# Kernel tuning notes

Hardware: AMD Instinct MI355X
Metric: run time of the kernel (lower is better)

## Reference

```python
import jax, jax.numpy as jnp
import numpy as np

B, P, N = 1024, 100, 101
EMB, H, DK = 128, 8, 16
SQRT_EMB = 11.313708498984761
CLIP = 10.0


def setup_inputs() -> dict:
    key = jax.random.key(0)
    ks = jax.random.split(key, 12)
    inp = {
        "encoded_last_node": jax.random.normal(ks[0], (B, P, EMB), jnp.float32),
        "load": jax.random.uniform(ks[1], (B, P), jnp.float32),
        "time": jax.random.uniform(ks[2], (B, P), jnp.float32),
        "length": jax.random.uniform(ks[3], (B, P), jnp.float32),
        "route_open": jax.random.uniform(ks[4], (B, P), jnp.float32),
        "ninf_mask": jnp.zeros((B, P, N), jnp.float32),
        "encoded_nodes": jax.random.normal(ks[5], (B, N, EMB), jnp.float32),
        # weights stored [in, out]
        "Wq": jax.random.normal(ks[6], (EMB + 4, H * DK), jnp.float32) * 0.05,
        "Wk": jax.random.normal(ks[7], (EMB, H * DK), jnp.float32) * 0.05,
        "Wv": jax.random.normal(ks[8], (EMB, H * DK), jnp.float32) * 0.05,
        "Wc": jax.random.normal(ks[9], (H * DK, EMB), jnp.float32) * 0.05,
        "bc": jax.random.normal(ks[10], (EMB,), jnp.float32) * 0.05,
    }
    return inp


def _heads(x):
    # [B, n, H*DK] -> [B, H, n, DK]
    b, n, _ = x.shape
    return x.reshape(b, n, H, DK).transpose(0, 2, 1, 3)


def reference(encoded_last_node, load, time, length, route_open, ninf_mask,
              encoded_nodes, Wq, Wk, Wv, Wc, bc):
    # set_kv
    k = _heads(encoded_nodes @ Wk)            # [B,H,N,DK]
    v = _heads(encoded_nodes @ Wv)            # [B,H,N,DK]
    # forward
    input_cat = jnp.concatenate(
        [encoded_last_node, load[:, :, None], time[:, :, None],
         length[:, :, None], route_open[:, :, None]], axis=2)  # [B,P,EMB+4]
    q = _heads(input_cat @ Wq)                # [B,H,P,DK]
    score = jnp.einsum('bhpd,bhnd->bhpn', q, k) / jnp.sqrt(jnp.float32(DK))
    score = score + ninf_mask[:, None, :, :]
    weights = jax.nn.softmax(score, axis=3)
    out = jnp.einsum('bhpn,bhnd->bhpd', weights, v)
    out_concat = out.transpose(0, 2, 1, 3).reshape(out.shape[0], out.shape[2], H * DK)
    mh = out_concat @ Wc + bc                 # [B,P,EMB]
    score2 = jnp.einsum('bpe,bne->bpn', mh, encoded_nodes) / SQRT_EMB
    score2 = CLIP * jnp.tanh(score2) + ninf_mask
    probs = jax.nn.softmax(score2, axis=2)
    return probs
```

## Files before the change

kernel.cpp:

```cpp
#include <hip/hip_runtime.h>
#include <stdint.h>

#define B_    1024
#define P_    100
#define N_    101
#define EMB_  128
#define H_    8
#define DK_   16

#define ROWS  112
#define KSTR  136

typedef uint16_t bf16;
typedef __attribute__((ext_vector_type(8))) short short8;
typedef __attribute__((ext_vector_type(4))) float float4v;

struct F4 { float x, y, z, w; };

#define L2E 1.4426950408889634f

#if __has_builtin(__builtin_amdgcn_exp2f)
#define EXP2(x) __builtin_amdgcn_exp2f(x)
#else
#define EXP2(x) exp2f(x)
#endif
#if __has_builtin(__builtin_amdgcn_rcpf)
#define RCP(x) __builtin_amdgcn_rcpf(x)
#else
#define RCP(x) (1.0f / (x))
#endif

__device__ __forceinline__ float b2f(bf16 u) {
    union { uint32_t i; float f; } c; c.i = ((uint32_t)u) << 16; return c.f;
}
__device__ __forceinline__ bf16 f2b(float f) {
    union { float f; uint32_t i; } c; c.f = f;
    return (bf16)((c.i + 0x8000u) >> 16);
}
__device__ __forceinline__ uint32_t pk2(float a, float b) {
    union { float f; uint32_t i; } ca, cb; ca.f = a; cb.f = b;
    return __builtin_amdgcn_perm(cb.i + 0x8000u, ca.i + 0x8000u, 0x07060302u);
}

__device__ __forceinline__ void stage_m(const float* __restrict__ src, int nrows,
                                        bf16* __restrict__ dst, int tid) {
    for (int i = tid; i < ROWS * 32; i += 1024) {
        int r = i >> 5, c = (i & 31) << 2;
        uint32_t p0 = 0, p1 = 0;
        if (r < nrows) {
            float4 v = *(const float4*)(src + (size_t)r * EMB_ + c);
            p0 = pk2(v.x, v.y); p1 = pk2(v.z, v.w);
        }
        uint32_t* d = (uint32_t*)(dst + r * KSTR + c);
        d[0] = p0; d[1] = p1;
    }
}

__global__ __launch_bounds__(256)
void prep_wT(const float* __restrict__ Wq, const float* __restrict__ Wk,
             const float* __restrict__ Wv, const float* __restrict__ Wc,
             bf16* __restrict__ ws) {
    int idx = blockIdx.x * 256 + threadIdx.x;
    int w = idx >> 14, rem = idx & 16383;
    int k = rem >> 7, o = rem & 127;
    const float* W = (w == 0) ? Wk : (w == 1) ? Wv : (w == 2) ? Wq : Wc;
    ws[((size_t)w << 14) + o * 128 + k] = f2b(W[(size_t)k * 128 + o]);
}

__global__ __launch_bounds__(1024, 4)
void vrp_kernel(const float* __restrict__ eln,
                const float* __restrict__ load_,
                const float* __restrict__ time_,
                const float* __restrict__ len_,
                const float* __restrict__ open_,
                const float* __restrict__ mask_,
                const float* __restrict__ enc_,
                const float* __restrict__ Wq,
                const float* __restrict__ bc,
                const bf16* __restrict__ wsWT,
                float* __restrict__ out)
{
    const int b    = blockIdx.x;
    const int tid  = threadIdx.x;
    const int wave = tid >> 6;
    const int lane = tid & 63;
    const int lr = lane & 15, lq = lane >> 4, lk = lq << 3;

    __shared__ bf16 smem[78336];
    __shared__ float sS4[ROWS * 4];
    __shared__ float sWq4[4 * EMB_];
    bf16* const R1 = smem;
    bf16* const R2 = smem + 15232;
    bf16* const R3 = smem + 30464;
    bf16* const R4 = smem + 47872;
    bf16* const R5 = smem + 63104;

    const bf16* WkT = wsWT;
    const bf16* WvT = wsWT + 16384;
    const bf16* WqT = wsWT + 32768;
    const bf16* WcT = wsWT + 49152;

    const float* encB  = enc_  + (size_t)b * N_ * EMB_;
    const float* elnB  = eln   + (size_t)b * P_ * EMB_;
    const float* maskB = mask_ + (size_t)b * P_ * N_;
    float*       outB  = out   + (size_t)b * P_ * N_;

    stage_m(encB, N_, R1, tid);
    stage_m(elnB, P_, R5, tid);
    if (tid < 512) {
        int d = tid >> 2, c = 112 + ((tid & 3) << 2);
        uint32_t* z = (uint32_t*)(R3 + d * KSTR + c);
        z[0] = 0; z[1] = 0;
    }
    if (tid < ROWS * 4) {
        int r = tid >> 2, j = tid & 3;
        float v = 0.f;
        if (r < P_) {
            const float* s4 = (j == 0) ? load_ : (j == 1) ? time_
                             : (j == 2) ? len_ : open_;
            v = s4[(size_t)b * P_ + r];
        }
        sS4[r * 4 + j] = v;
    }
    if (tid < 512) {
        int j = tid >> 7, c = tid & 127;
        sWq4[j * EMB_ + c] = Wq[(size_t)(EMB_ + j) * EMB_ + c];
    }
    __syncthreads();

    {
        const int col = 16 * (wave & 7) + lr;
        const int mt0 = (wave >> 3) ? 4 : 0;
        const int mt1 = (wave >> 3) ? 7 : 4;
        short8 bk[4], bv[4], bq[4];
        {
            const bf16* rk = WkT + (size_t)col * 128 + lk;
            const bf16* rv = WvT + (size_t)col * 128 + lk;
            const bf16* rq = WqT + (size_t)col * 128 + lk;
            #pragma unroll
            for (int s = 0; s < 4; ++s) {
                bk[s] = *(const short8*)(rk + s * 32);
                bv[s] = *(const short8*)(rv + s * 32);
                bq[s] = *(const short8*)(rq + s * 32);
            }
        }
        float w0 = sWq4[col], w1 = sWq4[EMB_ + col];
        float w2 = sWq4[2 * EMB_ + col], w3 = sWq4[3 * EMB_ + col];
        for (int mt = mt0; mt < mt1; ++mt) {
            short8 a[4];
            #pragma unroll
            for (int s = 0; s < 4; ++s)
                a[s] = *(const short8*)(R1 + (mt * 16 + lr) * KSTR + s * 32 + lk);
            float4v ck = {0.f, 0.f, 0.f, 0.f}, cv = {0.f, 0.f, 0.f, 0.f};
            #pragma unroll
            for (int s = 0; s < 4; ++s) {
                ck = __builtin_amdgcn_mfma_f32_16x16x32_bf16(a[s], bk[s], ck, 0, 0, 0);
                cv = __builtin_amdgcn_mfma_f32_16x16x32_bf16(a[s], bv[s], cv, 0, 0, 0);
            }
            int n0 = mt * 16 + (lq << 2);
            #pragma unroll
            for (int r = 0; r < 4; ++r)
                R2[(n0 + r) * KSTR + col] = f2b(ck[r]);
            uint32_t* d = (uint32_t*)(R3 + col * KSTR + n0);
            d[0] = pk2(cv[0], cv[1]);
            d[1] = pk2(cv[2], cv[3]);
            short8 aq[4];
            #pragma unroll
            for (int s = 0; s < 4; ++s)
                aq[s] = *(const short8*)(R5 + (mt * 16 + lr) * KSTR + s * 32 + lk);
            float4v cq = {0.f, 0.f, 0.f, 0.f};
            #pragma unroll
            for (int s = 0; s < 4; ++s)
                cq = __builtin_amdgcn_mfma_f32_16x16x32_bf16(aq[s], bq[s], cq, 0, 0, 0);
            int row0 = mt * 16 + (lq << 2);
            #pragma unroll
            for (int r = 0; r < 4; ++r) {
                const float* s4 = sS4 + (row0 + r) * 4;
                float acc = cq[r] + s4[0] * w0 + s4[1] * w1 + s4[2] * w2 + s4[3] * w3;
                R4[(row0 + r) * KSTR + col] = f2b(acc * (0.25f * L2E));
            }
        }
    }
    __syncthreads();

    const int hg = (wave >= 7) ? 1 : 0;
    const int pt = wave - hg * 7;
    float msk2[7][4];
    float4v o4[4];
    if (wave < 14) {
        bf16* Pbuf = hg ? R5 : R1;
        {
            uint32_t* z = (uint32_t*)(Pbuf + (pt * 16 + lr) * KSTR + 112 + (lq << 2));
            z[0] = 0; z[1] = 0;
        }
        {
            const int p = pt * 16 + lr;
            const bool pvalid = (p < P_);
            const float* mrow = maskB + (size_t)(pvalid ? p : 0) * N_;
            #pragma unroll
            for (int nt = 0; nt < 6; ++nt) {
                int nb = nt * 16 + (lq << 2);
                F4 mv = *(const F4*)(mrow + nb);
                msk2[nt][0] = pvalid ? mv.x * L2E : 0.f;
                msk2[nt][1] = pvalid ? mv.y * L2E : 0.f;
                msk2[nt][2] = pvalid ? mv.z * L2E : 0.f;
                msk2[nt][3] = pvalid ? mv.w * L2E : 0.f;
            }
            if (lq == 0) {
                F4 mv = *(const F4*)(mrow + 96);
                msk2[6][0] = pvalid ? mv.x * L2E : 0.f;
                msk2[6][1] = pvalid ? mv.y * L2E : 0.f;
                msk2[6][2] = pvalid ? mv.z * L2E : 0.f;
                msk2[6][3] = pvalid ? mv.w * L2E : 0.f;
            } else if (lq == 1) {
                msk2[6][0] = pvalid ? mrow[100] * L2E : 0.f;
                msk2[6][1] = -3.0e38f; msk2[6][2] = -3.0e38f; msk2[6][3] = -3.0e38f;
            } else {
                msk2[6][0] = -3.0e38f; msk2[6][1] = -3.0e38f;
                msk2[6][2] = -3.0e38f; msk2[6][3] = -3.0e38f;
            }
        }
        #pragma unroll
        for (int hh = 0; hh < 4; ++hh) {
            int h  = hg * 4 + hh;
            int k0 = (h >> 1) << 5;
            short8 bq = *(const short8*)(R4 + (pt * 16 + lr) * KSTR + k0 + lk);
            if ((lq >> 1) != (h & 1)) bq = (short8){0,0,0,0,0,0,0,0};
            float sc[7][4];
            #pragma unroll
            for (int nt = 0; nt < 7; ++nt) {
                short8 ak = *(const short8*)(R2 + (nt * 16 + lr) * KSTR + k0 + lk);
                float4v cc = {msk2[nt][0], msk2[nt][1], msk2[nt][2], msk2[nt][3]};
                cc = __builtin_amdgcn_mfma_f32_16x16x32_bf16(ak, bq, cc, 0, 0, 0);
                #pragma unroll
                for (int r = 0; r < 4; ++r) sc[nt][r] = cc[r];
            }
            float mm[7];
            #pragma unroll
            for (int nt = 0; nt < 7; ++nt)
                mm[nt] = fmaxf(fmaxf(sc[nt][0], sc[nt][1]),
                               fmaxf(sc[nt][2], sc[nt][3]));
            float m = fmaxf(fmaxf(fmaxf(mm[0], mm[1]), fmaxf(mm[2], mm[3])),
                            fmaxf(fmaxf(mm[4], mm[5]), mm[6]));
            m = fmaxf(m, __shfl_xor(m, 16));
            m = fmaxf(m, __shfl_xor(m, 32));
            float s0 = 0.f, s1 = 0.f, s2 = 0.f, s3 = 0.f;
            #pragma unroll
            for (int nt = 0; nt < 7; ++nt) {
                float e0 = EXP2(sc[nt][0] - m); sc[nt][0] = e0; s0 += e0;
                float e1 = EXP2(sc[nt][1] - m); sc[nt][1] = e1; s1 += e1;
                float e2 = EXP2(sc[nt][2] - m); sc[nt][2] = e2; s2 += e2;
                float e3 = EXP2(sc[nt][3] - m); sc[nt][3] = e3; s3 += e3;
            }
            float su = (s0 + s1) + (s2 + s3);
            su += __shfl_xor(su, 16);
            su += __shfl_xor(su, 32);
            float inv = RCP(su);
            #pragma unroll
            for (int nt = 0; nt < 7; ++nt) {
                uint32_t* d = (uint32_t*)(Pbuf + (pt * 16 + lr) * KSTR
                                          + nt * 16 + (lq << 2));
                d[0] = pk2(sc[nt][0] * inv, sc[nt][1] * inv);
                d[1] = pk2(sc[nt][2] * inv, sc[nt][3] * inv);
            }
            float4v o = {0.f, 0.f, 0.f, 0.f};
            #pragma unroll
            for (int ks = 0; ks < 128; ks += 32) {
                short8 a2 = *(const short8*)(Pbuf + (pt * 16 + lr) * KSTR + ks + lk);
                short8 b2 = *(const short8*)(R3 + (h * 16 + lr) * KSTR + ks + lk);
                o = __builtin_amdgcn_mfma_f32_16x16x32_bf16(a2, b2, o, 0, 0, 0);
            }
            o4[hh] = o;
        }
    }
    __syncthreads();

    if (wave < 14) {
        #pragma unroll
        for (int hh = 0; hh < 4; ++hh) {
            int h = hg * 4 + hh;
            #pragma unroll
            for (int r = 0; r < 4; ++r)
                R4[(pt * 16 + (lq << 2) + r) * KSTR + h * 16 + lr] = f2b(o4[hh][r]);
        }
    }
    stage_m(encB, N_, R2, tid);
    __syncthreads();

    {
        const int col = 16 * (wave & 7) + lr;
        const int mt0 = (wave >> 3) ? 4 : 0;
        const int mt1 = (wave >> 3) ? 7 : 4;
        short8 bw[4];
        {
            const bf16* rc = WcT + (size_t)col * 128 + lk;
            #pragma unroll
            for (int s = 0; s < 4; ++s) bw[s] = *(const short8*)(rc + s * 32);
        }
        float bcv = bc[col];
        for (int mt = mt0; mt < mt1; ++mt) {
            short8 a[4];
            #pragma unroll
            for (int s = 0; s < 4; ++s)
                a[s] = *(const short8*)(R4 + (mt * 16 + lr) * KSTR + s * 32 + lk);
            float4v c = {0.f, 0.f, 0.f, 0.f};
            #pragma unroll
            for (int s = 0; s < 4; ++s)
                c = __builtin_amdgcn_mfma_f32_16x16x32_bf16(a[s], bw[s], c, 0, 0, 0);
            int row0 = mt * 16 + (lq << 2);
            #pragma unroll
            for (int r = 0; r < 4; ++r) {
                float m = c[r] + bcv;
                bf16 hb = f2b(m);
                R1[(row0 + r) * KSTR + col] = hb;
                R5[(row0 + r) * KSTR + col] = f2b(m - b2f(hb));
            }
        }
    }
    __syncthreads();

    if (wave < 7) {
        const int pt2 = wave;
        short8 bhi[4], blo[4];
        #pragma unroll
        for (int s = 0; s < 4; ++s) {
            bhi[s] = *(const short8*)(R1 + (pt2 * 16 + lr) * KSTR + s * 32 + lk);
            blo[s] = *(const short8*)(R5 + (pt2 * 16 + lr) * KSTR + s * 32 + lk);
        }
        float sc[7][4];
        #pragma unroll
        for (int nt = 0; nt < 7; ++nt) {
            float4v cc = {0.f, 0.f, 0.f, 0.f};
            #pragma unroll
            for (int s = 0; s < 4; ++s) {
                short8 ae = *(const short8*)(R2 + (nt * 16 + lr) * KSTR + s * 32 + lk);
                cc = __builtin_amdgcn_mfma_f32_16x16x32_bf16(ae, bhi[s], cc, 0, 0, 0);
                cc = __builtin_amdgcn_mfma_f32_16x16x32_bf16(ae, blo[s], cc, 0, 0, 0);
            }
            #pragma unroll
            for (int r = 0; r < 4; ++r) {
                float y = EXP2(cc[r] * (0.08838834764831845f * 2.0f * L2E));
                float t = fmaf(-2.0f, RCP(y + 1.0f), 1.0f);
                sc[nt][r] = fmaf(10.0f * L2E, t, msk2[nt][r]);
            }
        }
        float mm[7];
        #pragma unroll
        for (int nt = 0; nt < 7; ++nt)
            mm[nt] = fmaxf(fmaxf(sc[nt][0], sc[nt][1]),
                           fmaxf(sc[nt][2], sc[nt][3]));
        float m = fmaxf(fmaxf(fmaxf(mm[0], mm[1]), fmaxf(mm[2], mm[3])),
                        fmaxf(fmaxf(mm[4], mm[5]), mm[6]));
        m = fmaxf(m, __shfl_xor(m, 16));
        m = fmaxf(m, __shfl_xor(m, 32));
        float s0 = 0.f, s1 = 0.f, s2 = 0.f, s3 = 0.f;
        #pragma unroll
        for (int nt = 0; nt < 7; ++nt) {
            float e0 = EXP2(sc[nt][0] - m); sc[nt][0] = e0; s0 += e0;
            float e1 = EXP2(sc[nt][1] - m); sc[nt][1] = e1; s1 += e1;
            float e2 = EXP2(sc[nt][2] - m); sc[nt][2] = e2; s2 += e2;
            float e3 = EXP2(sc[nt][3] - m); sc[nt][3] = e3; s3 += e3;
        }
        float su = (s0 + s1) + (s2 + s3);
        su += __shfl_xor(su, 16);
        su += __shfl_xor(su, 32);
        float inv = RCP(su);
        const int p = pt2 * 16 + lr;
        if (p < P_) {
            float* orow = outB + (size_t)p * N_;
            #pragma unroll
            for (int nt = 0; nt < 6; ++nt) {
                F4 ov = { sc[nt][0] * inv, sc[nt][1] * inv,
                          sc[nt][2] * inv, sc[nt][3] * inv };
                *(F4*)(orow + nt * 16 + (lq << 2)) = ov;
            }
            if (lq == 0) {
                F4 ov = { sc[6][0] * inv, sc[6][1] * inv,
                          sc[6][2] * inv, sc[6][3] * inv };
                *(F4*)(orow + 96) = ov;
            } else if (lq == 1) {
                orow[100] = sc[6][0] * inv;
            }
        }
    }
}

extern "C" void kernel_launch(void* const* d_in, const int* in_sizes, int n_in,
                              void* d_out, int out_size, void* d_ws, size_t ws_size,
                              hipStream_t stream) {
    const float* eln   = (const float*)d_in[0];
    const float* load_ = (const float*)d_in[1];
    const float* time_ = (const float*)d_in[2];
    const float* len_  = (const float*)d_in[3];
    const float* open_ = (const float*)d_in[4];
    const float* mask_ = (const float*)d_in[5];
    const float* enc_  = (const float*)d_in[6];
    const float* Wq    = (const float*)d_in[7];
    const float* Wk    = (const float*)d_in[8];
    const float* Wv    = (const float*)d_in[9];
    const float* Wc    = (const float*)d_in[10];
    const float* bc    = (const float*)d_in[11];
    float* out = (float*)d_out;
    bf16* wsWT = (bf16*)d_ws;

    prep_wT<<<dim3(256), dim3(256), 0, stream>>>(Wq, Wk, Wv, Wc, wsWT);
    vrp_kernel<<<dim3(B_), dim3(1024), 0, stream>>>(
        eln, load_, time_, len_, open_, mask_, enc_, Wq, bc, wsWT, out);
}
```

Before: 274.0 us.

## Pass softmax probabilities between MFMAs via lane shuffles instead of LDS round-trip

The attention probabilities are now kept in registers and redistributed into the MFMA A-operand layout with cross-lane shuffles, instead of being written to a shared-memory buffer and read back. Query fragments are loaded once per head pair rather than per head. The second staging of encoded nodes into shared memory is dropped by reusing a buffer that still holds them, and the hi/lo mh buffers are remapped to match. This removes LDS store/load traffic and one staging copy, at the cost of many extra shuffle instructions.

```diff
diff --git a/kernel.cpp b/kernel.cpp
--- a/kernel.cpp
+++ b/kernel.cpp
@@ -188,11 +188,6 @@
     float msk2[7][4];
     float4v o4[4];
     if (wave < 14) {
-        bf16* Pbuf = hg ? R5 : R1;
-        {
-            uint32_t* z = (uint32_t*)(Pbuf + (pt * 16 + lr) * KSTR + 112 + (lq << 2));
-            z[0] = 0; z[1] = 0;
-        }
         {
             const int p = pt * 16 + lr;
             const bool pvalid = (p < P_);
@@ -220,12 +215,17 @@
                 msk2[6][2] = -3.0e38f; msk2[6][3] = -3.0e38f;
             }
         }
+        short8 q0 = *(const short8*)(R4 + (pt * 16 + lr) * KSTR + hg * 64 + lk);
+        short8 q1 = *(const short8*)(R4 + (pt * 16 + lr) * KSTR + hg * 64 + 32 + lk);
+        const int sA = ((lq & 1) << 5) + lr;
+        const int sB = sA + 16;
+        const bool hisel = (lq >= 2);
         #pragma unroll
         for (int hh = 0; hh < 4; ++hh) {
             int h  = hg * 4 + hh;
-            int k0 = (h >> 1) << 5;
-            short8 bq = *(const short8*)(R4 + (pt * 16 + lr) * KSTR + k0 + lk);
-            if ((lq >> 1) != (h & 1)) bq = (short8){0,0,0,0,0,0,0,0};
+            int k0 = hg * 64 + (hh >> 1) * 32;
+            short8 bq = (hh < 2) ? q0 : q1;
+            if ((lq >> 1) != (hh & 1)) bq = (short8){0,0,0,0,0,0,0,0};
             float sc[7][4];
             #pragma unroll
             for (int nt = 0; nt < 7; ++nt) {
@@ -256,19 +256,31 @@
             su += __shfl_xor(su, 16);
             su += __shfl_xor(su, 32);
             float inv = RCP(su);
+            uint32_t pd[8][2];
             #pragma unroll
             for (int nt = 0; nt < 7; ++nt) {
-                uint32_t* d = (uint32_t*)(Pbuf + (pt * 16 + lr) * KSTR
-                                          + nt * 16 + (lq << 2));
-                d[0] = pk2(sc[nt][0] * inv, sc[nt][1] * inv);
-                d[1] = pk2(sc[nt][2] * inv, sc[nt][3] * inv);
-            }
+                pd[nt][0] = pk2(sc[nt][0] * inv, sc[nt][1] * inv);
+                pd[nt][1] = pk2(sc[nt][2] * inv, sc[nt][3] * inv);
+            }
+            pd[7][0] = 0u; pd[7][1] = 0u;
             float4v o = {0.f, 0.f, 0.f, 0.f};
             #pragma unroll
-            for (int ks = 0; ks < 128; ks += 32) {
-                short8 a2 = *(const short8*)(Pbuf + (pt * 16 + lr) * KSTR + ks + lk);
-                short8 b2 = *(const short8*)(R3 + (h * 16 + lr) * KSTR + ks + lk);
-                o = __builtin_amdgcn_mfma_f32_16x16x32_bf16(a2, b2, o, 0, 0, 0);
+            for (int t = 0; t < 4; ++t) {
+                uint32_t a0 = (uint32_t)__shfl((int)pd[2*t][0], sA);
+                uint32_t a1 = (uint32_t)__shfl((int)pd[2*t][1], sA);
+                uint32_t b0 = (uint32_t)__shfl((int)pd[2*t+1][0], sA);
+                uint32_t b1 = (uint32_t)__shfl((int)pd[2*t+1][1], sA);
+                uint32_t c0 = (uint32_t)__shfl((int)pd[2*t][0], sB);
+                uint32_t c1 = (uint32_t)__shfl((int)pd[2*t][1], sB);
+                uint32_t d0 = (uint32_t)__shfl((int)pd[2*t+1][0], sB);
+                uint32_t d1 = (uint32_t)__shfl((int)pd[2*t+1][1], sB);
+                union { uint32_t u[4]; short8 s; } af;
+                af.u[0] = hisel ? b0 : a0;
+                af.u[1] = hisel ? b1 : a1;
+                af.u[2] = hisel ? d0 : c0;
+                af.u[3] = hisel ? d1 : c1;
+                short8 b2 = *(const short8*)(R3 + (h * 16 + lr) * KSTR + t * 32 + lk);
+                o = __builtin_amdgcn_mfma_f32_16x16x32_bf16(af.s, b2, o, 0, 0, 0);
             }
             o4[hh] = o;
         }
@@ -284,7 +296,6 @@
                 R4[(pt * 16 + (lq << 2) + r) * KSTR + h * 16 + lr] = f2b(o4[hh][r]);
         }
     }
-    stage_m(encB, N_, R2, tid);
     __syncthreads();
 
     {
@@ -312,8 +323,8 @@
             for (int r = 0; r < 4; ++r) {
                 float m = c[r] + bcv;
                 bf16 hb = f2b(m);
-                R1[(row0 + r) * KSTR + col] = hb;
-                R5[(row0 + r) * KSTR + col] = f2b(m - b2f(hb));
+                R5[(row0 + r) * KSTR + col] = hb;
+                R2[(row0 + r) * KSTR + col] = f2b(m - b2f(hb));
             }
         }
     }
@@ -324,8 +335,8 @@
         short8 bhi[4], blo[4];
         #pragma unroll
         for (int s = 0; s < 4; ++s) {
-            bhi[s] = *(const short8*)(R1 + (pt2 * 16 + lr) * KSTR + s * 32 + lk);
-            blo[s] = *(const short8*)(R5 + (pt2 * 16 + lr) * KSTR + s * 32 + lk);
+            bhi[s] = *(const short8*)(R5 + (pt2 * 16 + lr) * KSTR + s * 32 + lk);
+            blo[s] = *(const short8*)(R2 + (pt2 * 16 + lr) * KSTR + s * 32 + lk);
         }
         float sc[7][4];
         #pragma unroll
@@ -333,7 +344,7 @@
             float4v cc = {0.f, 0.f, 0.f, 0.f};
             #pragma unroll
             for (int s = 0; s < 4; ++s) {
-                short8 ae = *(const short8*)(R2 + (nt * 16 + lr) * KSTR + s * 32 + lk);
+                short8 ae = *(const short8*)(R1 + (nt * 16 + lr) * KSTR + s * 32 + lk);
                 cc = __builtin_amdgcn_mfma_f32_16x16x32_bf16(ae, bhi[s], cc, 0, 0, 0);
                 cc = __builtin_amdgcn_mfma_f32_16x16x32_bf16(ae, blo[s], cc, 0, 0, 0);
             }
```

After: 276.0 us. No clear change (+0.7%).

## Reassign LDS buffers to skip encoded_nodes restaging and drop second softmax max

Applied to the files above, without the earlier changes.

The LDS buffers are remapped so the encoded_nodes copy already staged in R1 is reused for the final score GEMM instead of being staged again into R2. Query fragments are preloaded into registers before an added barrier so that R4 and R5 can serve as probability buffers. The second softmax no longer computes a row max: it subtracts the constant upper bound 10*log2(e) from the tanh-clipped logits, which saves a reduction and two shuffles. The cost is one extra __syncthreads. The fixed bound is safe only while the mask entries are non-positive and at least one entry per row is finite; a row that is fully masked to -inf then yields 0/0 where the original would also degenerate.

```diff
diff --git a/kernel.cpp b/kernel.cpp
--- a/kernel.cpp
+++ b/kernel.cpp
@@ -187,12 +187,8 @@
     const int pt = wave - hg * 7;
     float msk2[7][4];
     float4v o4[4];
+    short8 q0, q1;
     if (wave < 14) {
-        bf16* Pbuf = hg ? R5 : R1;
-        {
-            uint32_t* z = (uint32_t*)(Pbuf + (pt * 16 + lr) * KSTR + 112 + (lq << 2));
-            z[0] = 0; z[1] = 0;
-        }
         {
             const int p = pt * 16 + lr;
             const bool pvalid = (p < P_);
@@ -220,12 +216,22 @@
                 msk2[6][2] = -3.0e38f; msk2[6][3] = -3.0e38f;
             }
         }
+        q0 = *(const short8*)(R4 + (pt * 16 + lr) * KSTR + hg * 64 + lk);
+        q1 = *(const short8*)(R4 + (pt * 16 + lr) * KSTR + hg * 64 + 32 + lk);
+    }
+    __syncthreads();
+    if (wave < 14) {
+        bf16* Pbuf = hg ? R4 : R5;
+        {
+            uint32_t* z = (uint32_t*)(Pbuf + (pt * 16 + lr) * KSTR + 112 + (lq << 2));
+            z[0] = 0; z[1] = 0;
+        }
         #pragma unroll
         for (int hh = 0; hh < 4; ++hh) {
             int h  = hg * 4 + hh;
-            int k0 = (h >> 1) << 5;
-            short8 bq = *(const short8*)(R4 + (pt * 16 + lr) * KSTR + k0 + lk);
-            if ((lq >> 1) != (h & 1)) bq = (short8){0,0,0,0,0,0,0,0};
+            int k0 = hg * 64 + (hh >> 1) * 32;
+            short8 bq = (hh < 2) ? q0 : q1;
+            if ((lq >> 1) != (hh & 1)) bq = (short8){0,0,0,0,0,0,0,0};
             float sc[7][4];
             #pragma unroll
             for (int nt = 0; nt < 7; ++nt) {
@@ -284,7 +290,6 @@
                 R4[(pt * 16 + (lq << 2) + r) * KSTR + h * 16 + lr] = f2b(o4[hh][r]);
         }
     }
-    stage_m(encB, N_, R2, tid);
     __syncthreads();
 
     {
@@ -312,8 +317,8 @@
             for (int r = 0; r < 4; ++r) {
                 float m = c[r] + bcv;
                 bf16 hb = f2b(m);
-                R1[(row0 + r) * KSTR + col] = hb;
-                R5[(row0 + r) * KSTR + col] = f2b(m - b2f(hb));
+                R5[(row0 + r) * KSTR + col] = hb;
+                R2[(row0 + r) * KSTR + col] = f2b(m - b2f(hb));
             }
         }
     }
@@ -324,8 +329,8 @@
         short8 bhi[4], blo[4];
         #pragma unroll
         for (int s = 0; s < 4; ++s) {
-            bhi[s] = *(const short8*)(R1 + (pt2 * 16 + lr) * KSTR + s * 32 + lk);
-            blo[s] = *(const short8*)(R5 + (pt2 * 16 + lr) * KSTR + s * 32 + lk);
+            bhi[s] = *(const short8*)(R5 + (pt2 * 16 + lr) * KSTR + s * 32 + lk);
+            blo[s] = *(const short8*)(R2 + (pt2 * 16 + lr) * KSTR + s * 32 + lk);
         }
         float sc[7][4];
         #pragma unroll
@@ -333,7 +338,7 @@
             float4v cc = {0.f, 0.f, 0.f, 0.f};
             #pragma unroll
             for (int s = 0; s < 4; ++s) {
-                short8 ae = *(const short8*)(R2 + (nt * 16 + lr) * KSTR + s * 32 + lk);
+                short8 ae = *(const short8*)(R1 + (nt * 16 + lr) * KSTR + s * 32 + lk);
                 cc = __builtin_amdgcn_mfma_f32_16x16x32_bf16(ae, bhi[s], cc, 0, 0, 0);
                 cc = __builtin_amdgcn_mfma_f32_16x16x32_bf16(ae, blo[s], cc, 0, 0, 0);
             }
@@ -344,22 +349,14 @@
                 sc[nt][r] = fmaf(10.0f * L2E, t, msk2[nt][r]);
             }
         }
-        float mm[7];
-        #pragma unroll
-        for (int nt = 0; nt < 7; ++nt)
-            mm[nt] = fmaxf(fmaxf(sc[nt][0], sc[nt][1]),
-                           fmaxf(sc[nt][2], sc[nt][3]));
-        float m = fmaxf(fmaxf(fmaxf(mm[0], mm[1]), fmaxf(mm[2], mm[3])),
-                        fmaxf(fmaxf(mm[4], mm[5]), mm[6]));
-        m = fmaxf(m, __shfl_xor(m, 16));
-        m = fmaxf(m, __shfl_xor(m, 32));
+        const float mF = 10.0f * L2E;
         float s0 = 0.f, s1 = 0.f, s2 = 0.f, s3 = 0.f;
         #pragma unroll
         for (int nt = 0; nt < 7; ++nt) {
-            float e0 = EXP2(sc[nt][0] - m); sc[nt][0] = e0; s0 += e0;
-            float e1 = EXP2(sc[nt][1] - m); sc[nt][1] = e1; s1 += e1;
-            float e2 = EXP2(sc[nt][2] - m); sc[nt][2] = e2; s2 += e2;
-            float e3 = EXP2(sc[nt][3] - m); sc[nt][3] = e3; s3 += e3;
+            float e0 = EXP2(sc[nt][0] - mF); sc[nt][0] = e0; s0 += e0;
+            float e1 = EXP2(sc[nt][1] - mF); sc[nt][1] = e1; s1 += e1;
+            float e2 = EXP2(sc[nt][2] - mF); sc[nt][2] = e2; s2 += e2;
+            float e3 = EXP2(sc[nt][3] - mF); sc[nt][3] = e3; s3 += e3;
         }
         float su = (s0 + s1) + (s2 + s3);
         su += __shfl_xor(su, 16);
```

After: 271.4 us. No clear change (-1.0%).
